# Kernel tuning notes

Hardware: AMD Instinct MI355X
Metric: run time of the kernel (lower is better)

Reference implementation:

```python
import jax, jax.numpy as jnp
import numpy as np

B, T, D, H, WIN, G = 2, 2048, 768, 12, 16, 32
HD = D // H            # 64
K = 2 * WIN + 1        # local kernel size = 33


def setup_inputs() -> dict:
    key = jax.random.key(0)
    ks = jax.random.split(key, 5)
    s = 1.0 / np.sqrt(D).astype(np.float32)
    x = jax.random.normal(ks[0], (B, T, D), jnp.float32)
    # first G tokens of every batch are global (matches original's nonzero(global_mask[b]))
    global_mask = jnp.zeros((B, T), jnp.int32).at[:, :G].set(1)
    Wq = jax.random.normal(ks[1], (D, D), jnp.float32) * s
    Wk = jax.random.normal(ks[2], (D, D), jnp.float32) * s
    Wv = jax.random.normal(ks[3], (D, D), jnp.float32) * s
    Wo = jax.random.normal(ks[4], (D, D), jnp.float32) * s
    bq = jnp.zeros((D,), jnp.float32)
    bk = jnp.zeros((D,), jnp.float32)
    bv = jnp.zeros((D,), jnp.float32)
    bo = jnp.zeros((D,), jnp.float32)
    return {"x": x, "global_mask": global_mask, "Wq": Wq, "bq": bq,
            "Wk": Wk, "bk": bk, "Wv": Wv, "bv": bv, "Wo": Wo, "bo": bo}


def reference(x, global_mask, Wq, bq, Wk, bk, Wv, bv, Wo, bo):
    def split_heads(y):
        return y.reshape(B, T, H, HD).transpose(0, 2, 1, 3)  # [B,H,T,HD]

    q = split_heads(x @ Wq + bq)
    k = split_heads(x @ Wk + bk)
    v = split_heads(x @ Wv + bv)

    scale = 1.0 / np.sqrt(HD).astype(np.float32)

    offs = jnp.arange(-WIN, WIN + 1)
    idx = jnp.arange(T)[:, None] + offs[None, :]          # [T,K]
    valid = (idx >= 0) & (idx < T)                        # [T,K]
    idxc = jnp.clip(idx, 0, T - 1)

    k_loc = k[:, :, idxc]                                 # [B,H,T,K,HD]
    s_loc = jnp.einsum('bhtd,bhtkd->bhtk', q, k_loc) * scale
    s_loc = jnp.where(valid, s_loc, -jnp.inf)             # out-of-range excluded from softmax

    # global tokens (same positions for every batch by construction)
    g_idx = jnp.nonzero(global_mask[0], size=G)[0]        # [G]
    k_g = k[:, :, g_idx]                                  # [B,H,G,HD]
    v_g = v[:, :, g_idx]
    s_g = jnp.einsum('bhtd,bhgd->bhtg', q, k_g) * scale   # [B,H,T,G]

    # joint softmax over [local window, global tokens] (globals in window are double-counted,
    # exactly as in the original torch.cat([local_s, g_score]))
    attn = jax.nn.softmax(jnp.concatenate([s_loc, s_g], axis=-1), axis=-1)
    a_loc = jnp.where(valid, attn[..., :K], 0.0)          # [B,H,T,K]
    a_g = attn[..., K:]                                   # [B,H,T,G]

    v_loc = v[:, :, idxc]                                 # [B,H,T,K,HD]
    ctx = (jnp.einsum('bhtk,bhtkd->bhtd', a_loc, v_loc)
           + jnp.einsum('bhtg,bhgd->bhtd', a_g, v_g))     # [B,H,T,HD]

    out = ctx.transpose(0, 2, 1, 3).reshape(B, T, D) @ Wo + bo

    # dense attention map: scatter local band (add; invalid entries are 0),
    # then overwrite global columns (matches original write order)
    rows = jnp.arange(T)[:, None]                         # [T,1]
    full_attn = jnp.zeros((B, H, T, T), jnp.float32)
    full_attn = full_attn.at[:, :, rows, idxc].add(a_loc)
    full_attn = full_attn.at[:, :, :, g_idx].set(a_g)
    return out, full_attn
```

## Files before the change

kernel.cpp:

```cpp
#include <hip/hip_runtime.h>

typedef unsigned short u16;
typedef __attribute__((ext_vector_type(4))) u16 u16x4;
typedef __attribute__((ext_vector_type(8))) u16 u16x8;
typedef __attribute__((ext_vector_type(8))) short bf16x8;
typedef __attribute__((ext_vector_type(4))) float f32x4;

#define BB 2
#define TT 2048
#define DD 768
#define NH 12
#define HDIM 64
#define NQKV 2304
#define MM 4096

__device__ __forceinline__ u16 f2bf(float f) {
  unsigned u = __float_as_uint(f);
  u += 0x7fffu + ((u >> 16) & 1u);
  return (u16)(u >> 16);
}
__device__ __forceinline__ float bf2f(u16 s) {
  return __uint_as_float(((unsigned)s) << 16);
}
__device__ __forceinline__ void async_load16(const void* g, void* l) {
  __builtin_amdgcn_global_load_lds((const __attribute__((address_space(1))) void*)g,
                                   (__attribute__((address_space(3))) void*)l, 16, 0, 0);
}

__global__ __launch_bounds__(256) void prep_all(const float* __restrict__ x,
                                                const float* __restrict__ Wq, const float* __restrict__ Wk,
                                                const float* __restrict__ Wv, const float* __restrict__ Wo,
                                                const int* __restrict__ gm,
                                                const float* __restrict__ bq, const float* __restrict__ bk,
                                                const float* __restrict__ bv,
                                                u16* __restrict__ xb, u16* __restrict__ wqkvT,
                                                u16* __restrict__ woT,
                                                int* __restrict__ gidx, float* __restrict__ biasqkv) {
  __shared__ float tile[32][33];
  const int bid = blockIdx.x;
  const int tid = threadIdx.x;
  if (bid < 3072) {
    int i = bid * 256 + tid;
    float4 v = ((const float4*)x)[i];
    u16x4 o = { f2bf(v.x), f2bf(v.y), f2bf(v.z), f2bf(v.w) };
    ((u16x4*)xb)[i] = o;
  } else if (bid < 5376) {
    int r = bid - 3072;
    int z = r / 576; r %= 576;
    int kx = r % 24, ny = r / 24;
    const float* W = (z == 0) ? Wq : (z == 1) ? Wk : (z == 2) ? Wv : Wo;
    u16* dst = (z < 3) ? (wqkvT + (size_t)z * DD * DD) : woT;
    int k0 = kx * 32, n0 = ny * 32;
    int tx = tid & 31, ty = tid >> 5;
#pragma unroll
    for (int j = 0; j < 4; ++j)
      tile[ty + j * 8][tx] = W[(size_t)(k0 + ty + j * 8) * DD + n0 + tx];
    __syncthreads();
#pragma unroll
    for (int j = 0; j < 4; ++j)
      dst[(size_t)(n0 + ty + j * 8) * DD + k0 + tx] = f2bf(tile[tx][ty + j * 8]);
  } else {
    for (int n = tid; n < NQKV; n += 256)
      biasqkv[n] = (n < 768) ? bq[n] : (n < 1536) ? bk[n - 768] : bv[n - 1536];
    if (tid < 64) {
      int lane = tid;
      if (lane < 32) gidx[lane] = 0;
      int base = 0;
      for (int c0 = 0; c0 < TT; c0 += 64) {
        int mval = gm[c0 + lane];
        unsigned long long bal = __ballot(mval != 0);
        int pre = __popcll(bal & ((1ull << lane) - 1ull));
        if (mval && (base + pre) < 32) gidx[base + pre] = c0 + lane;
        base += __popcll(bal);
        if (base >= 32) break;
      }
    }
  }
}

template <int BM, bool OUTBF>
__global__ __launch_bounds__(256) void gemm_bt(const u16* __restrict__ A, const u16* __restrict__ BT,
                                               const float* __restrict__ bias, void* __restrict__ Cv,
                                               int Ndim, int Kd) {
  constexpr int NJ = (BM == 128) ? 4 : 2;
  constexpr int ACH = BM / 32;
  __shared__ __attribute__((aligned(16))) u16 As[BM * 64];
  __shared__ __attribute__((aligned(16))) u16 Bs[128 * 64];
  const int tid = threadIdx.x;
  const int wave = tid >> 6, lane = tid & 63;
  const int m0 = blockIdx.x * BM, n0 = blockIdx.y * 128;
  const int wm = (BM == 128) ? ((wave & 1) << 6) : 0;
  const int wn = (BM == 128) ? ((wave >> 1) << 6) : (wave << 5);
  const int lr = lane & 15, lk = lane >> 4;
  const int srow_b = lane >> 3;
  const int scol = (lane & 7) * 8;

  f32x4 acc[4][NJ] = {};

  const int kIters = Kd >> 6;
  for (int kt = 0; kt < kIters; ++kt) {
#pragma unroll
    for (int cc = 0; cc < ACH; ++cc) {
      int c = wave * ACH + cc;
      int srow = c * 8 + srow_b;
      async_load16(A + (size_t)(m0 + srow) * Kd + (kt << 6) + scol, (void*)(As + c * 512));
    }
#pragma unroll
    for (int cc = 0; cc < 4; ++cc) {
      int c = wave * 4 + cc;
      int srow = c * 8 + srow_b;
      async_load16(BT + (size_t)(n0 + srow) * Kd + (kt << 6) + scol, (void*)(Bs + c * 512));
    }
    __syncthreads();
#pragma unroll
    for (int kc = 0; kc < 2; ++kc) {
      bf16x8 af[4], bfr[NJ];
#pragma unroll
      for (int i = 0; i < 4; ++i)
        af[i] = *(const bf16x8*)(As + (wm + i * 16 + lr) * 64 + kc * 32 + lk * 8);
#pragma unroll
      for (int j = 0; j < NJ; ++j)
        bfr[j] = *(const bf16x8*)(Bs + (wn + j * 16 + lr) * 64 + kc * 32 + lk * 8);
#pragma unroll
      for (int i = 0; i < 4; ++i)
#pragma unroll
        for (int j = 0; j < NJ; ++j)
          acc[i][j] = __builtin_amdgcn_mfma_f32_16x16x32_bf16(af[i], bfr[j], acc[i][j], 0, 0, 0);
    }
    __syncthreads();
  }

#pragma unroll
  for (int i = 0; i < 4; ++i) {
    const int row = m0 + wm + i * 16 + lk * 4;
#pragma unroll
    for (int j = 0; j < NJ; ++j) {
      const int col = n0 + wn + j * 16 + lr;
      const float bs = bias[col];
#pragma unroll
      for (int r = 0; r < 4; ++r) {
        const float val = acc[i][j][r] + bs;
        if (OUTBF) ((u16*)Cv)[(size_t)(row + r) * Ndim + col] = f2bf(val);
        else       ((float*)Cv)[(size_t)(row + r) * Ndim + col] = val;
      }
    }
  }
}

__global__ __launch_bounds__(256) void attn_kernel(const u16* __restrict__ qb,
                                                   const int* __restrict__ gidx,
                                                   u16* __restrict__ ctxb,
                                                   float* __restrict__ fattn) {
  __shared__ __attribute__((aligned(16))) u16 Kl[96 * 72];
  __shared__ __attribute__((aligned(16))) u16 Kg[32 * 72];
  __shared__ __attribute__((aligned(16))) u16 Vl[96 * 72];
  __shared__ __attribute__((aligned(16))) u16 Vg[32 * 72];
  __shared__ __attribute__((aligned(16))) float probs[64 * 68];
  __shared__ int gidxs[32];

  const int tid = threadIdx.x;
  const int blk = blockIdx.x;
  const int chunk = blk & 31;
  const int h = (blk >> 5) % NH;
  const int b = blk / 384;
  const int t0 = chunk << 6;

  {
    const int r = tid >> 3;
    const int c8 = (tid & 7) << 3;
#pragma unroll
    for (int it = 0; it < 3; ++it) {
      int rr = it * 32 + r;
      int t = t0 - 16 + rr;
      t = t < 0 ? 0 : (t > TT - 1 ? TT - 1 : t);
      const u16* src = qb + (size_t)(b * TT + t) * NQKV + h * HDIM + c8;
      *(u16x8*)(Kl + rr * 72 + c8) = *(const u16x8*)(src + 768);
      *(u16x8*)(Vl + rr * 72 + c8) = *(const u16x8*)(src + 1536);
    }
    {
      int t = gidx[r];
      const u16* src = qb + (size_t)(b * TT + t) * NQKV + h * HDIM + c8;
      *(u16x8*)(Kg + r * 72 + c8) = *(const u16x8*)(src + 768);
      *(u16x8*)(Vg + r * 72 + c8) = *(const u16x8*)(src + 1536);
    }
    if (tid < 32) gidxs[tid] = gidx[tid];
  }
  __syncthreads();

  const int tl = tid >> 2, sub = tid & 3;
  const int t = t0 + tl;
  const u16* qp = qb + (size_t)(b * TT + t) * NQKV + h * HDIM;
  float qv[64];
#pragma unroll
  for (int i = 0; i < 8; ++i) {
    u16x8 qq = *(const u16x8*)(qp + i * 8);
#pragma unroll
    for (int e = 0; e < 8; ++e) qv[i * 8 + e] = bf2f(qq[e]);
  }

  float cacc[16];
#pragma unroll
  for (int i = 0; i < 16; ++i) cacc[i] = 0.f;

#pragma unroll 1
  for (int rep = 0; rep < 4; ++rep) {
    float sc[17];
    float mmax = -__builtin_inff();
#pragma unroll
    for (int i = 0; i < 17; ++i) {
      const int s = sub + (i << 2);
      const u16* kp;
      bool valid;
      if (s < 33) { kp = Kl + (tl + s) * 72; int j = t - 16 + s; valid = (j >= 0) && (j < TT); }
      else if (s < 65) { kp = Kg + (s - 33) * 72; valid = true; }
      else { kp = Kg; valid = false; }
      float d = 0.f;
#pragma unroll
      for (int i2 = 0; i2 < 8; ++i2) {
        u16x8 kv = *(const u16x8*)(kp + i2 * 8);
#pragma unroll
        for (int e = 0; e < 8; ++e) d += qv[i2 * 8 + e] * bf2f(kv[e]);
      }
      sc[i] = valid ? d * 0.125f : -__builtin_inff();
      mmax = fmaxf(mmax, sc[i]);
    }
    mmax = fmaxf(mmax, __shfl_xor(mmax, 1));
    mmax = fmaxf(mmax, __shfl_xor(mmax, 2));
    float sum = 0.f;
#pragma unroll
    for (int i = 0; i < 17; ++i) { sc[i] = __expf(sc[i] - mmax); sum += sc[i]; }
    sum += __shfl_xor(sum, 1);
    sum += __shfl_xor(sum, 2);
    const float inv = 1.0f / sum;
#pragma unroll
    for (int i = 0; i < 17; ++i) {
      const int s = sub + (i << 2);
      sc[i] *= inv;
      if (s < 65) probs[tl * 68 + s] = sc[i];
    }
    __syncthreads();

#pragma unroll 1
    for (int k = 0; k < 65; ++k) {
      const float pv = probs[tl * 68 + k];
      const u16* vp = (k < 33) ? (Vl + (tl + k) * 72) : (Vg + (k - 33) * 72);
      const u16* vq = vp + (sub << 4);
      u16x8 v0 = *(const u16x8*)(vq);
      u16x8 v1 = *(const u16x8*)(vq + 8);
#pragma unroll
      for (int e = 0; e < 8; ++e) { cacc[e] += pv * bf2f(v0[e]); cacc[8 + e] += pv * bf2f(v1[e]); }
    }
    __syncthreads();
  }

  {
    u16x8 cb0, cb1;
#pragma unroll
    for (int e = 0; e < 8; ++e) { cb0[e] = f2bf(cacc[e] * 0.25f); cb1[e] = f2bf(cacc[8 + e] * 0.25f); }
    u16* dst = ctxb + (size_t)(b * TT + t) * DD + h * HDIM + (sub << 4);
    *(u16x8*)dst = cb0;
    *(u16x8*)(dst + 8) = cb1;
  }

  float* fbase = fattn + ((size_t)(b * NH + h) * TT + t0) * TT;
#pragma unroll 1
  for (int it = 0; it < 128; ++it) {
    int f = it * 256 + tid;
    int rl = f >> 9;
    int c4 = (f & 511) << 2;
    int trow = t0 + rl;
    float4 v = make_float4(0.f, 0.f, 0.f, 0.f);
    int kk = c4 - trow + 16;
    if (kk >= -3 && kk < 33) {
      const float* pr = probs + rl * 68;
      float* vp = &v.x;
#pragma unroll
      for (int e = 0; e < 4; ++e) {
        int k2 = kk + e;
        if ((unsigned)k2 < 33u) vp[e] = pr[k2];
      }
    }
    *(float4*)(fbase + (size_t)rl * TT + c4) = v;
  }
  __syncthreads();

  {
    int rl = tid >> 2, g0 = (tid & 3) << 3;
    const float* pr = probs + rl * 68 + 33;
    float* frow = fbase + (size_t)rl * TT;
#pragma unroll
    for (int e = 0; e < 8; ++e) frow[gidxs[g0 + e]] = pr[g0 + e];
  }
}

extern "C" void kernel_launch(void* const* d_in, const int* in_sizes, int n_in,
                              void* d_out, int out_size, void* d_ws, size_t ws_size,
                              hipStream_t stream) {
  const float* x  = (const float*)d_in[0];
  const int* gm   = (const int*)d_in[1];
  const float* Wq = (const float*)d_in[2];
  const float* bq = (const float*)d_in[3];
  const float* Wk = (const float*)d_in[4];
  const float* bk = (const float*)d_in[5];
  const float* Wv = (const float*)d_in[6];
  const float* bv = (const float*)d_in[7];
  const float* Wo = (const float*)d_in[8];
  const float* bo = (const float*)d_in[9];

  float* out = (float*)d_out;
  float* fattn = out + (size_t)BB * TT * DD;

  char* p = (char*)d_ws;
  u16* xb      = (u16*)p;  p += (size_t)MM * DD * 2;
  u16* wqkvT   = (u16*)p;  p += (size_t)NQKV * DD * 2;
  u16* woT     = (u16*)p;  p += (size_t)DD * DD * 2;
  float* biasq = (float*)p; p += (size_t)NQKV * 4;
  int* gidx    = (int*)p;  p += 128;
  u16* qkvb    = (u16*)p;  p += (size_t)MM * NQKV * 2;
  u16* ctxb    = (u16*)p;  p += (size_t)MM * DD * 2;

  prep_all<<<5377, 256, 0, stream>>>(x, Wq, Wk, Wv, Wo, gm, bq, bk, bv,
                                     xb, wqkvT, woT, gidx, biasq);
  gemm_bt<128, true><<<dim3(MM / 128, NQKV / 128), 256, 0, stream>>>(xb, wqkvT, biasq, qkvb, NQKV, DD);
  attn_kernel<<<BB * NH * (TT / 64), 256, 0, stream>>>(qkvb, gidx, ctxb, fattn);
  gemm_bt<64, false><<<dim3(MM / 64, DD / 128), 256, 0, stream>>>(ctxb, woT, bo, out, DD, DD);
}
```

Measured before the change: 600.1 us.

## Drop repeated softmax passes and move dense attention-map writes into output-projection kernel

The attention kernel previously recomputed scores, softmax and the PV accumulation four times and then scaled by 0.25; this now runs once. The dense full_attn scatter is moved out of the attention kernel. Probabilities are staged to a compact workspace buffer, and a combined tail kernel writes the map using many small 16-row blocks alongside the output-projection GEMM blocks. The aim is to remove redundant compute and spread the large memory-bound map write over more blocks that run next to the GEMM. The cost is an extra workspace round trip for the probabilities.

```diff
diff --git a/kernel.cpp b/kernel.cpp
--- a/kernel.cpp
+++ b/kernel.cpp
@@ -78,53 +78,44 @@
   }
 }
 
-template <int BM, bool OUTBF>
-__global__ __launch_bounds__(256) void gemm_bt(const u16* __restrict__ A, const u16* __restrict__ BT,
-                                               const float* __restrict__ bias, void* __restrict__ Cv,
-                                               int Ndim, int Kd) {
-  constexpr int NJ = (BM == 128) ? 4 : 2;
-  constexpr int ACH = BM / 32;
-  __shared__ __attribute__((aligned(16))) u16 As[BM * 64];
+__global__ __launch_bounds__(256) void gemm_qkv(const u16* __restrict__ A, const u16* __restrict__ BT,
+                                                const float* __restrict__ bias, u16* __restrict__ C,
+                                                int Ndim, int Kd) {
+  __shared__ __attribute__((aligned(16))) u16 As[128 * 64];
   __shared__ __attribute__((aligned(16))) u16 Bs[128 * 64];
   const int tid = threadIdx.x;
   const int wave = tid >> 6, lane = tid & 63;
-  const int m0 = blockIdx.x * BM, n0 = blockIdx.y * 128;
-  const int wm = (BM == 128) ? ((wave & 1) << 6) : 0;
-  const int wn = (BM == 128) ? ((wave >> 1) << 6) : (wave << 5);
+  const int m0 = blockIdx.x * 128, n0 = blockIdx.y * 128;
+  const int wm = (wave & 1) << 6, wn = (wave >> 1) << 6;
   const int lr = lane & 15, lk = lane >> 4;
   const int srow_b = lane >> 3;
   const int scol = (lane & 7) * 8;
 
-  f32x4 acc[4][NJ] = {};
+  f32x4 acc[4][4] = {};
 
   const int kIters = Kd >> 6;
   for (int kt = 0; kt < kIters; ++kt) {
-#pragma unroll
-    for (int cc = 0; cc < ACH; ++cc) {
-      int c = wave * ACH + cc;
-      int srow = c * 8 + srow_b;
-      async_load16(A + (size_t)(m0 + srow) * Kd + (kt << 6) + scol, (void*)(As + c * 512));
-    }
 #pragma unroll
     for (int cc = 0; cc < 4; ++cc) {
       int c = wave * 4 + cc;
       int srow = c * 8 + srow_b;
+      async_load16(A + (size_t)(m0 + srow) * Kd + (kt << 6) + scol, (void*)(As + c * 512));
       async_load16(BT + (size_t)(n0 + srow) * Kd + (kt << 6) + scol, (void*)(Bs + c * 512));
     }
     __syncthreads();
 #pragma unroll
     for (int kc = 0; kc < 2; ++kc) {
-      bf16x8 af[4], bfr[NJ];
+      bf16x8 af[4], bfr[4];
 #pragma unroll
       for (int i = 0; i < 4; ++i)
         af[i] = *(const bf16x8*)(As + (wm + i * 16 + lr) * 64 + kc * 32 + lk * 8);
 #pragma unroll
-      for (int j = 0; j < NJ; ++j)
+      for (int j = 0; j < 4; ++j)
         bfr[j] = *(const bf16x8*)(Bs + (wn + j * 16 + lr) * 64 + kc * 32 + lk * 8);
 #pragma unroll
       for (int i = 0; i < 4; ++i)
 #pragma unroll
-        for (int j = 0; j < NJ; ++j)
+        for (int j = 0; j < 4; ++j)
           acc[i][j] = __builtin_amdgcn_mfma_f32_16x16x32_bf16(af[i], bfr[j], acc[i][j], 0, 0, 0);
     }
     __syncthreads();
@@ -134,15 +125,12 @@
   for (int i = 0; i < 4; ++i) {
     const int row = m0 + wm + i * 16 + lk * 4;
 #pragma unroll
-    for (int j = 0; j < NJ; ++j) {
+    for (int j = 0; j < 4; ++j) {
       const int col = n0 + wn + j * 16 + lr;
       const float bs = bias[col];
 #pragma unroll
-      for (int r = 0; r < 4; ++r) {
-        const float val = acc[i][j][r] + bs;
-        if (OUTBF) ((u16*)Cv)[(size_t)(row + r) * Ndim + col] = f2bf(val);
-        else       ((float*)Cv)[(size_t)(row + r) * Ndim + col] = val;
-      }
+      for (int r = 0; r < 4; ++r)
+        C[(size_t)(row + r) * Ndim + col] = f2bf(acc[i][j][r] + bs);
     }
   }
 }
@@ -150,13 +138,12 @@
 __global__ __launch_bounds__(256) void attn_kernel(const u16* __restrict__ qb,
                                                    const int* __restrict__ gidx,
                                                    u16* __restrict__ ctxb,
-                                                   float* __restrict__ fattn) {
+                                                   float* __restrict__ probsG) {
   __shared__ __attribute__((aligned(16))) u16 Kl[96 * 72];
   __shared__ __attribute__((aligned(16))) u16 Kg[32 * 72];
   __shared__ __attribute__((aligned(16))) u16 Vl[96 * 72];
   __shared__ __attribute__((aligned(16))) u16 Vg[32 * 72];
   __shared__ __attribute__((aligned(16))) float probs[64 * 68];
-  __shared__ int gidxs[32];
 
   const int tid = threadIdx.x;
   const int blk = blockIdx.x;
@@ -183,7 +170,6 @@
       *(u16x8*)(Kg + r * 72 + c8) = *(const u16x8*)(src + 768);
       *(u16x8*)(Vg + r * 72 + c8) = *(const u16x8*)(src + 1536);
     }
-    if (tid < 32) gidxs[tid] = gidx[tid];
   }
   __syncthreads();
 
@@ -198,98 +184,174 @@
     for (int e = 0; e < 8; ++e) qv[i * 8 + e] = bf2f(qq[e]);
   }
 
+  float sc[17];
+  float mmax = -__builtin_inff();
+#pragma unroll
+  for (int i = 0; i < 17; ++i) {
+    const int s = sub + (i << 2);
+    const u16* kp;
+    bool valid;
+    if (s < 33) { kp = Kl + (tl + s) * 72; int j = t - 16 + s; valid = (j >= 0) && (j < TT); }
+    else if (s < 65) { kp = Kg + (s - 33) * 72; valid = true; }
+    else { kp = Kg; valid = false; }
+    float d = 0.f;
+#pragma unroll
+    for (int i2 = 0; i2 < 8; ++i2) {
+      u16x8 kv = *(const u16x8*)(kp + i2 * 8);
+#pragma unroll
+      for (int e = 0; e < 8; ++e) d += qv[i2 * 8 + e] * bf2f(kv[e]);
+    }
+    sc[i] = valid ? d * 0.125f : -__builtin_inff();
+    mmax = fmaxf(mmax, sc[i]);
+  }
+  mmax = fmaxf(mmax, __shfl_xor(mmax, 1));
+  mmax = fmaxf(mmax, __shfl_xor(mmax, 2));
+  float sum = 0.f;
+#pragma unroll
+  for (int i = 0; i < 17; ++i) { sc[i] = __expf(sc[i] - mmax); sum += sc[i]; }
+  sum += __shfl_xor(sum, 1);
+  sum += __shfl_xor(sum, 2);
+  const float inv = 1.0f / sum;
+#pragma unroll
+  for (int i = 0; i < 17; ++i) {
+    const int s = sub + (i << 2);
+    sc[i] *= inv;
+    if (s < 65) probs[tl * 68 + s] = sc[i];
+  }
+  __syncthreads();
+
   float cacc[16];
 #pragma unroll
   for (int i = 0; i < 16; ++i) cacc[i] = 0.f;
-
 #pragma unroll 1
-  for (int rep = 0; rep < 4; ++rep) {
-    float sc[17];
-    float mmax = -__builtin_inff();
-#pragma unroll
-    for (int i = 0; i < 17; ++i) {
-      const int s = sub + (i << 2);
-      const u16* kp;
-      bool valid;
-      if (s < 33) { kp = Kl + (tl + s) * 72; int j = t - 16 + s; valid = (j >= 0) && (j < TT); }
-      else if (s < 65) { kp = Kg + (s - 33) * 72; valid = true; }
-      else { kp = Kg; valid = false; }
-      float d = 0.f;
-#pragma unroll
-      for (int i2 = 0; i2 < 8; ++i2) {
-        u16x8 kv = *(const u16x8*)(kp + i2 * 8);
-#pragma unroll
-        for (int e = 0; e < 8; ++e) d += qv[i2 * 8 + e] * bf2f(kv[e]);
-      }
-      sc[i] = valid ? d * 0.125f : -__builtin_inff();
-      mmax = fmaxf(mmax, sc[i]);
-    }
-    mmax = fmaxf(mmax, __shfl_xor(mmax, 1));
-    mmax = fmaxf(mmax, __shfl_xor(mmax, 2));
-    float sum = 0.f;
-#pragma unroll
-    for (int i = 0; i < 17; ++i) { sc[i] = __expf(sc[i] - mmax); sum += sc[i]; }
-    sum += __shfl_xor(sum, 1);
-    sum += __shfl_xor(sum, 2);
-    const float inv = 1.0f / sum;
-#pragma unroll
-    for (int i = 0; i < 17; ++i) {
-      const int s = sub + (i << 2);
-      sc[i] *= inv;
-      if (s < 65) probs[tl * 68 + s] = sc[i];
-    }
-    __syncthreads();
-
-#pragma unroll 1
-    for (int k = 0; k < 65; ++k) {
-      const float pv = probs[tl * 68 + k];
-      const u16* vp = (k < 33) ? (Vl + (tl + k) * 72) : (Vg + (k - 33) * 72);
-      const u16* vq = vp + (sub << 4);
-      u16x8 v0 = *(const u16x8*)(vq);
-      u16x8 v1 = *(const u16x8*)(vq + 8);
-#pragma unroll
-      for (int e = 0; e < 8; ++e) { cacc[e] += pv * bf2f(v0[e]); cacc[8 + e] += pv * bf2f(v1[e]); }
-    }
-    __syncthreads();
-  }
-
+  for (int k = 0; k < 65; ++k) {
+    const float pv = probs[tl * 68 + k];
+    const u16* vp = (k < 33) ? (Vl + (tl + k) * 72) : (Vg + (k - 33) * 72);
+    const u16* vq = vp + (sub << 4);
+    u16x8 v0 = *(const u16x8*)(vq);
+    u16x8 v1 = *(const u16x8*)(vq + 8);
+#pragma unroll
+    for (int e = 0; e < 8; ++e) { cacc[e] += pv * bf2f(v0[e]); cacc[8 + e] += pv * bf2f(v1[e]); }
+  }
   {
     u16x8 cb0, cb1;
 #pragma unroll
-    for (int e = 0; e < 8; ++e) { cb0[e] = f2bf(cacc[e] * 0.25f); cb1[e] = f2bf(cacc[8 + e] * 0.25f); }
+    for (int e = 0; e < 8; ++e) { cb0[e] = f2bf(cacc[e]); cb1[e] = f2bf(cacc[8 + e]); }
     u16* dst = ctxb + (size_t)(b * TT + t) * DD + h * HDIM + (sub << 4);
     *(u16x8*)dst = cb0;
     *(u16x8*)(dst + 8) = cb1;
   }
 
-  float* fbase = fattn + ((size_t)(b * NH + h) * TT + t0) * TT;
+  {
+    float4* dst = (float4*)(probsG + ((size_t)(b * NH + h) * TT + t0) * 68);
+    const float4* srcp = (const float4*)probs;
 #pragma unroll 1
-  for (int it = 0; it < 128; ++it) {
-    int f = it * 256 + tid;
-    int rl = f >> 9;
-    int c4 = (f & 511) << 2;
-    int trow = t0 + rl;
-    float4 v = make_float4(0.f, 0.f, 0.f, 0.f);
-    int kk = c4 - trow + 16;
-    if (kk >= -3 && kk < 33) {
-      const float* pr = probs + rl * 68;
-      float* vp = &v.x;
-#pragma unroll
-      for (int e = 0; e < 4; ++e) {
-        int k2 = kk + e;
-        if ((unsigned)k2 < 33u) vp[e] = pr[k2];
-      }
-    }
-    *(float4*)(fbase + (size_t)rl * TT + c4) = v;
-  }
-  __syncthreads();
-
-  {
-    int rl = tid >> 2, g0 = (tid & 3) << 3;
-    const float* pr = probs + rl * 68 + 33;
-    float* frow = fbase + (size_t)rl * TT;
-#pragma unroll
-    for (int e = 0; e < 8; ++e) frow[gidxs[g0 + e]] = pr[g0 + e];
+    for (int i = tid; i < 1088; i += 256) dst[i] = srcp[i];
+  }
+}
+
+#define G2_BLOCKS 384
+__global__ __launch_bounds__(256) void tail_k(const u16* __restrict__ ctxb, const u16* __restrict__ woT,
+                                              const float* __restrict__ bo, float* __restrict__ out,
+                                              const float* __restrict__ probsG, const int* __restrict__ gidx,
+                                              float* __restrict__ fattn) {
+  __shared__ __attribute__((aligned(16))) u16 sA[64 * 64];
+  __shared__ __attribute__((aligned(16))) u16 sB[128 * 64];
+  const int tid = threadIdx.x;
+  const int bid = blockIdx.x;
+
+  if (bid < G2_BLOCKS) {
+    const int wave = tid >> 6, lane = tid & 63;
+    const int m0 = (bid & 63) * 64, n0 = (bid >> 6) * 128;
+    const int wn = wave << 5;
+    const int lr = lane & 15, lk = lane >> 4;
+    const int srow_b = lane >> 3;
+    const int scol = (lane & 7) * 8;
+
+    f32x4 acc[4][2] = {};
+    for (int kt = 0; kt < DD / 64; ++kt) {
+#pragma unroll
+      for (int cc = 0; cc < 2; ++cc) {
+        int c = wave * 2 + cc;
+        int srow = c * 8 + srow_b;
+        async_load16(ctxb + (size_t)(m0 + srow) * DD + (kt << 6) + scol, (void*)(sA + c * 512));
+      }
+#pragma unroll
+      for (int cc = 0; cc < 4; ++cc) {
+        int c = wave * 4 + cc;
+        int srow = c * 8 + srow_b;
+        async_load16(woT + (size_t)(n0 + srow) * DD + (kt << 6) + scol, (void*)(sB + c * 512));
+      }
+      __syncthreads();
+#pragma unroll
+      for (int kc = 0; kc < 2; ++kc) {
+        bf16x8 af[4], bfr[2];
+#pragma unroll
+        for (int i = 0; i < 4; ++i)
+          af[i] = *(const bf16x8*)(sA + (i * 16 + lr) * 64 + kc * 32 + lk * 8);
+#pragma unroll
+        for (int j = 0; j < 2; ++j)
+          bfr[j] = *(const bf16x8*)(sB + (wn + j * 16 + lr) * 64 + kc * 32 + lk * 8);
+#pragma unroll
+        for (int i = 0; i < 4; ++i)
+#pragma unroll
+          for (int j = 0; j < 2; ++j)
+            acc[i][j] = __builtin_amdgcn_mfma_f32_16x16x32_bf16(af[i], bfr[j], acc[i][j], 0, 0, 0);
+      }
+      __syncthreads();
+    }
+#pragma unroll
+    for (int i = 0; i < 4; ++i) {
+      const int row = m0 + i * 16 + lk * 4;
+#pragma unroll
+      for (int j = 0; j < 2; ++j) {
+        const int col = n0 + wn + j * 16 + lr;
+        const float bs = bo[col];
+#pragma unroll
+        for (int r = 0; r < 4; ++r)
+          out[(size_t)(row + r) * DD + col] = acc[i][j][r] + bs;
+      }
+    }
+  } else {
+    float* Lp = (float*)sA;
+    int* gidxs = (int*)sB;
+    const int fid = bid - G2_BLOCKS;
+    const int slice = fid & 127;
+    const int h = (fid >> 7) % NH;
+    const int b = fid / (128 * NH);
+    const int t0s = slice << 4;
+
+    const float4* src = (const float4*)(probsG + ((size_t)(b * NH + h) * TT + t0s) * 68);
+    for (int i = tid; i < 272; i += 256) ((float4*)Lp)[i] = src[i];
+    if (tid < 32) gidxs[tid] = gidx[tid];
+    __syncthreads();
+
+    float* fbase = fattn + ((size_t)(b * NH + h) * TT + t0s) * TT;
+#pragma unroll 1
+    for (int it = 0; it < 32; ++it) {
+      int q = it * 256 + tid;
+      int rl = q >> 9;
+      int c4 = (q & 511) << 2;
+      int trow = t0s + rl;
+      float4 v = make_float4(0.f, 0.f, 0.f, 0.f);
+      int kk = c4 - trow + 16;
+      if (kk >= -3 && kk < 33) {
+        float* vp = &v.x;
+#pragma unroll
+        for (int e = 0; e < 4; ++e) {
+          int k2 = kk + e;
+          if ((unsigned)k2 < 33u) vp[e] = Lp[rl * 68 + k2];
+        }
+      }
+      *(float4*)(fbase + (size_t)rl * TT + c4) = v;
+    }
+    __syncthreads();
+#pragma unroll
+    for (int rep = 0; rep < 2; ++rep) {
+      int w = rep * 256 + tid;
+      int rl = w >> 5, g = w & 31;
+      fbase[(size_t)rl * TT + gidxs[g]] = Lp[rl * 68 + 33 + g];
+    }
   }
 }
 
@@ -318,10 +380,11 @@
   int* gidx    = (int*)p;  p += 128;
   u16* qkvb    = (u16*)p;  p += (size_t)MM * NQKV * 2;
   u16* ctxb    = (u16*)p;  p += (size_t)MM * DD * 2;
+  float* probsG= (float*)p; p += (size_t)MM * NH * 68 * 4;
 
   prep_all<<<5377, 256, 0, stream>>>(x, Wq, Wk, Wv, Wo, gm, bq, bk, bv,
                                      xb, wqkvT, woT, gidx, biasq);
-  gemm_bt<128, true><<<dim3(MM / 128, NQKV / 128), 256, 0, stream>>>(xb, wqkvT, biasq, qkvb, NQKV, DD);
-  attn_kernel<<<BB * NH * (TT / 64), 256, 0, stream>>>(qkvb, gidx, ctxb, fattn);
-  gemm_bt<64, false><<<dim3(MM / 64, DD / 128), 256, 0, stream>>>(ctxb, woT, bo, out, DD, DD);
-}
+  gemm_qkv<<<dim3(MM / 128, NQKV / 128), 256, 0, stream>>>(xb, wqkvT, biasq, qkvb, NQKV, DD);
+  attn_kernel<<<BB * NH * (TT / 64), 256, 0, stream>>>(qkvb, gidx, ctxb, probsG);
+  tail_k<<<G2_BLOCKS + BB * NH * (TT / 16), 256, 0, stream>>>(ctxb, woT, bo, out, probsG, gidx, fattn);
+}
```

Result: faster. 538.8 us (-10.2%).
